# Kernel optimization log

Measured on AMD Instinct MI355X. Metric: run time of the kernel, lower is better.

## Reference

```python
import jax, jax.numpy as jnp
import numpy as np
from jax import lax

B = 8
N = 460800          # anchors per image
PRE = 2000          # pre_nms_top_n
POST = 1000         # post_nms_top_n
NMS_T = 0.7
MIN_SIZE = 1e-3
IMG_H = 1024.0
IMG_W = 1024.0
BBOX_XFORM_CLIP = float(np.log(1000.0 / 16.0))


def setup_inputs() -> dict:
    key = jax.random.key(0)
    k1, k2, k3, k4 = jax.random.split(key, 4)
    # plausible anchors: centers in image, sizes 16..256
    ctr = jax.random.uniform(k1, (N, 2), minval=0.0, maxval=1024.0)
    wh = jax.random.uniform(k2, (N, 2), minval=16.0, maxval=256.0)
    anchors = jnp.concatenate([ctr - 0.5 * wh, ctr + 0.5 * wh], axis=-1)
    objectness = jax.random.normal(k3, (B, N), dtype=jnp.float32)
    bbox_deltas = jax.random.normal(k4, (B, N, 4), dtype=jnp.float32) * 0.1
    return {"anchors": anchors, "objectness": objectness, "bbox_deltas": bbox_deltas}


def _decode(deltas, anchors):
    # BoxCoder.decode with weights (1,1,1,1)
    w = anchors[..., 2] - anchors[..., 0]
    h = anchors[..., 3] - anchors[..., 1]
    cx = anchors[..., 0] + 0.5 * w
    cy = anchors[..., 1] + 0.5 * h
    dx, dy = deltas[..., 0], deltas[..., 1]
    dw = jnp.minimum(deltas[..., 2], BBOX_XFORM_CLIP)
    dh = jnp.minimum(deltas[..., 3], BBOX_XFORM_CLIP)
    pcx = dx * w + cx
    pcy = dy * h + cy
    pw = jnp.exp(dw) * w
    ph = jnp.exp(dh) * h
    return jnp.stack([pcx - 0.5 * pw, pcy - 0.5 * ph,
                      pcx + 0.5 * pw, pcy + 0.5 * ph], axis=-1)


def _nms_keep(boxes, valid):
    # boxes: [PRE,4] sorted by descending score; greedy NMS keep mask
    area = (boxes[:, 2] - boxes[:, 0]) * (boxes[:, 3] - boxes[:, 1])
    lt = jnp.maximum(boxes[:, None, :2], boxes[None, :, :2])
    rb = jnp.minimum(boxes[:, None, 2:], boxes[None, :, 2:])
    whi = jnp.clip(rb - lt, 0.0)
    inter = whi[..., 0] * whi[..., 1]          # [PRE,PRE]
    iou = inter / (area[:, None] + area[None, :] - inter)
    idx = jnp.arange(PRE)

    def body(i, keep):
        sup = keep[i] & (iou[i] > NMS_T) & (idx > i)
        return keep & ~sup

    return lax.fori_loop(0, PRE, body, valid)


def _per_image(proposals, scores):
    # top pre_nms_top_n by raw objectness (returned sorted descending)
    top_scores, idx = lax.top_k(scores, PRE)
    b = proposals[idx]                          # [PRE,4]
    # clip to image
    x1 = jnp.clip(b[:, 0], 0.0, IMG_W)
    y1 = jnp.clip(b[:, 1], 0.0, IMG_H)
    x2 = jnp.clip(b[:, 2], 0.0, IMG_W)
    y2 = jnp.clip(b[:, 3], 0.0, IMG_H)
    b = jnp.stack([x1, y1, x2, y2], axis=-1)
    # remove small boxes (mask instead of drop, jit-friendly)
    small = (x2 - x1 < MIN_SIZE) | (y2 - y1 < MIN_SIZE)
    keep = _nms_keep(b, ~small)
    s = jnp.where(keep, top_scores, -jnp.inf)
    _, fidx = lax.top_k(s, POST)
    return b[fidx]                              # [POST,4]


def reference(anchors, objectness, bbox_deltas):
    proposals = _decode(bbox_deltas, anchors[None])   # [B,N,4]
    boxes = jax.vmap(_per_image)(proposals, objectness)  # [B,POST,4]
    return boxes
```

## Files before the change

kernel.cpp:

```cpp
#include <hip/hip_runtime.h>
#include <stdint.h>

#define B 8
#define N 460800
#define NV4 115200
#define PRE 2000
#define POST 1000
#define CAP 4096
#define NBIN 4096
#define RANKP 2048
#define NWORD 32
#define NMS_T 0.7f
#define XCLIP 4.135166556742356

#define SCAN_BLOCKS 45
#define SCAN_ITER 10
#define SCAN_STRIDE (SCAN_BLOCKS * 256)

typedef unsigned long long u64;

__device__ __forceinline__ uint32_t fkey(float f) {
    uint32_t u = __float_as_uint(f);
    return (u & 0x80000000u) ? ~u : (u | 0x80000000u);
}

__device__ __forceinline__ u64 readlane_u64(u64 v, int lane) {
    uint32_t lo = __builtin_amdgcn_readlane((uint32_t)v, lane);
    uint32_t hi = __builtin_amdgcn_readlane((uint32_t)(v >> 32), lane);
    return ((u64)hi << 32) | lo;
}

#define ZBYTES 131328
__global__ __launch_bounds__(256) void k_zero(uint4* __restrict__ p) {
    int i = blockIdx.x * 256 + threadIdx.x;
    if (i < ZBYTES / 16) p[i] = make_uint4(0u, 0u, 0u, 0u);
}

__global__ __launch_bounds__(256) void k_hist(const float4* __restrict__ obj4,
                                              uint32_t* __restrict__ hist) {
    __shared__ uint32_t lh[2][NBIN];
    int b = blockIdx.y;
    for (int i = threadIdx.x; i < NBIN; i += 256) { lh[0][i] = 0; lh[1][i] = 0; }
    __syncthreads();
    const float4* s = obj4 + (size_t)b * NV4;
    int t0 = blockIdx.x * 256 + threadIdx.x;
    uint32_t* h = lh[threadIdx.x & 1];
    float4 v[SCAN_ITER];
#pragma unroll
    for (int k = 0; k < SCAN_ITER; ++k) v[k] = s[t0 + k * SCAN_STRIDE];
#pragma unroll
    for (int k = 0; k < SCAN_ITER; ++k) {
        atomicAdd(&h[fkey(v[k].x) >> 20], 1u);
        atomicAdd(&h[fkey(v[k].y) >> 20], 1u);
        atomicAdd(&h[fkey(v[k].z) >> 20], 1u);
        atomicAdd(&h[fkey(v[k].w) >> 20], 1u);
    }
    __syncthreads();
    uint32_t* gh = hist + (size_t)b * NBIN;
    for (int i = threadIdx.x; i < NBIN; i += 256) {
        uint32_t s2 = lh[0][i] + lh[1][i];
        if (s2) atomicAdd(&gh[i], s2);
    }
}

#define LBUF 2048
__global__ __launch_bounds__(256) void k_compact(const float4* __restrict__ obj4,
                                                 const uint32_t* __restrict__ hist,
                                                 uint32_t* __restrict__ cnt,
                                                 u64* __restrict__ cand) {
    __shared__ u64 buf[LBUF];
    __shared__ uint32_t lcnt, base, cutsh;
    int b = blockIdx.y;
    if (threadIdx.x == 0) lcnt = 0;
    if (threadIdx.x < 64) {
        int lane = threadIdx.x;
        const uint32_t* h = hist + (size_t)b * NBIN;
        uint32_t gs = 0;
        for (int t = 0; t < 64; ++t) gs += h[lane * 64 + t];
        uint32_t suf = gs;
        for (int d = 1; d < 64; d <<= 1) {
            uint32_t vv = __shfl_down(suf, d);
            if (lane + d < 64) suf += vv;
        }
        unsigned long long m = __ballot(suf >= PRE);
        int G = 63 - __clzll(m);
        uint32_t A = 0;
        if (G < 63) A = __shfl(suf, G + 1);
        uint32_t hv = h[G * 64 + lane];
        uint32_t suf2 = hv;
        for (int d = 1; d < 64; d <<= 1) {
            uint32_t vv = __shfl_down(suf2, d);
            if (lane + d < 64) suf2 += vv;
        }
        unsigned long long m2 = __ballot(A + suf2 >= PRE);
        int t2 = 63 - __clzll(m2);
        if (lane == 0) cutsh = (uint32_t)(G * 64 + t2);
    }
    __syncthreads();
    uint32_t cb = cutsh;
    const float4* s = obj4 + (size_t)b * NV4;
    int t0 = blockIdx.x * 256 + threadIdx.x;
    float4 v[SCAN_ITER];
#pragma unroll
    for (int k = 0; k < SCAN_ITER; ++k) v[k] = s[t0 + k * SCAN_STRIDE];
#pragma unroll
    for (int k = 0; k < SCAN_ITER; ++k) {
        int i4 = (t0 + k * SCAN_STRIDE) * 4;
        float fv[4] = {v[k].x, v[k].y, v[k].z, v[k].w};
#pragma unroll
        for (int c = 0; c < 4; ++c) {
            uint32_t key = fkey(fv[c]);
            if ((key >> 20) >= cb) {
                uint32_t p = atomicAdd(&lcnt, 1u);
                u64 e = ((u64)key << 32) | (uint32_t)(~(uint32_t)(i4 + c));
                if (p < LBUF) buf[p] = e;
                else {
                    uint32_t g = atomicAdd(&cnt[b], 1u);
                    if (g < CAP) cand[(size_t)b * CAP + g] = e;
                }
            }
        }
    }
    __syncthreads();
    uint32_t nb = lcnt < LBUF ? lcnt : LBUF;
    if (threadIdx.x == 0) base = atomicAdd(&cnt[b], nb);
    __syncthreads();
    uint32_t bs = base;
    for (uint32_t t = threadIdx.x; t < nb; t += 256) {
        uint32_t g = bs + t;
        if (g < CAP) cand[(size_t)b * CAP + g] = buf[t];
    }
}

__global__ __launch_bounds__(64) void k_rankdec(const uint32_t* __restrict__ cnt,
                                                const u64* __restrict__ cand,
                                                const float4* __restrict__ anchors,
                                                const float4* __restrict__ deltas,
                                                float4* __restrict__ boxes,
                                                uint32_t* __restrict__ occ) {
    int b = blockIdx.x;
    int lane = threadIdx.x;
    int slot = blockIdx.y * 64 + lane;
    uint32_t n = cnt[b]; if (n > CAP) n = CAP;
    const u64* C = cand + (size_t)b * CAP;
    u64 mykey = (slot < (int)n) ? C[slot] : 0ull;
    int ng = ((int)n + 63) >> 6;
    auto ld = [&](int g) -> u64 {
        int j = g * 64 + lane;
        int jc = j < (CAP - 1) ? j : (CAP - 1);
        u64 kv = C[jc];
        return (j < (int)n) ? kv : 0ull;
    };
    u64 kv0 = ld(0), kv1 = ld(1), kv2 = ld(2);
    int r0 = 0, r1 = 0;
    for (int g = 0; g < ng; ++g) {
        u64 kvn = ld(g + 3);
#pragma unroll
        for (int t = 0; t < 64; t += 2) {
            u64 ka = readlane_u64(kv0, t);
            u64 kb = readlane_u64(kv0, t + 1);
            r0 += (ka > mykey) ? 1 : 0;
            r1 += (kb > mykey) ? 1 : 0;
        }
        kv0 = kv1; kv1 = kv2; kv2 = kvn;
    }
    int r = r0 + r1;
    int rank = (slot < (int)n) ? r : slot;
    if (rank < RANKP) {
        float4 outb = make_float4(0.f, 0.f, 0.f, 0.f);
        if (slot < (int)n && rank < PRE) {
            uint32_t idx = ~(uint32_t)mykey;
            if (idx < N) {
                float4 a = anchors[idx];
                float4 d = deltas[(size_t)b * N + idx];
                float w = a.z - a.x, h = a.w - a.y;
                float cx = a.x + 0.5f * w, cy = a.y + 0.5f * h;
                float dw = fminf(d.z, (float)XCLIP);
                float dh = fminf(d.w, (float)XCLIP);
                float pcx = d.x * w + cx, pcy = d.y * h + cy;
                float pw = expf(dw) * w, ph = expf(dh) * h;
                float x1 = pcx - 0.5f * pw, y1 = pcy - 0.5f * ph;
                float x2 = pcx + 0.5f * pw, y2 = pcy + 0.5f * ph;
                x1 = fminf(fmaxf(x1, 0.f), 1024.f);
                y1 = fminf(fmaxf(y1, 0.f), 1024.f);
                x2 = fminf(fmaxf(x2, 0.f), 1024.f);
                y2 = fminf(fmaxf(y2, 0.f), 1024.f);
                outb = make_float4(x1, y1, x2, y2);
            }
        }
        boxes[(size_t)b * RANKP + rank] = outb;
        occ[(size_t)b * RANKP + rank] = 0u;
    }
}

#define NTRI (NWORD * (NWORD + 1) / 2)
__global__ void k_mask(const float4* __restrict__ boxes, u64* __restrict__ adj,
                       uint32_t* __restrict__ occ, u64* __restrict__ valid) {
    int b = blockIdx.x;
    int L = blockIdx.y;
    int tw = 0, rem = L;
    while (rem >= NWORD - tw) { rem -= NWORD - tw; ++tw; }
    int tr = tw + rem;
    __shared__ float4 jb[64];
    __shared__ float ja[64];
    int t = threadIdx.x;
    const float4* bx = boxes + (size_t)b * RANKP;
    float4 v = bx[tw * 64 + t];
    jb[t] = v;
    ja[t] = (v.z - v.x) * (v.w - v.y);
    int i = tr * 64 + t;
    float4 bi = bx[i];
    float ai = (bi.z - bi.x) * (bi.w - bi.y);
    __syncthreads();
    u64 word = 0;
    for (int kk = 0; kk < 64; ++kk) {
        int j = tw * 64 + kk;
        float4 bj = jb[kk];
        float xx1 = fmaxf(bi.x, bj.x), yy1 = fmaxf(bi.y, bj.y);
        float xx2 = fminf(bi.z, bj.z), yy2 = fminf(bi.w, bj.w);
        float iw = fmaxf(xx2 - xx1, 0.f), ih = fmaxf(yy2 - yy1, 0.f);
        float inter = iw * ih;
        float iou = inter / (ai + ja[kk] - inter);
        if (j < i && iou > NMS_T) word |= 1ull << kk;
    }
    __builtin_nontemporal_store(word, &adj[((size_t)b * RANKP + i) * NWORD + tw]);
    if (word) atomicOr(&occ[(size_t)b * RANKP + i], 1u << tw);
    if (tw == tr) {
        bool ok = !((bi.z - bi.x < 1e-3f) || (bi.w - bi.y < 1e-3f));
        u64 bal = __ballot(ok);
        if (t == 0) valid[(size_t)b * NWORD + tr] = bal;
    }
}

__global__ __launch_bounds__(64, 1) void k_nms(const u64* __restrict__ valid,
                                               const u64* __restrict__ adj,
                                               const uint32_t* __restrict__ occ,
                                               const float4* __restrict__ boxes,
                                               float4* __restrict__ out) {
    int b = blockIdx.x;
    int lane = threadIdx.x;
    const u64* AdjG = adj + (size_t)b * RANKP * NWORD;
    const uint32_t* OccG = occ + (size_t)b * RANKP;
    uint32_t o[NWORD];
#pragma unroll
    for (int g = 0; g < NWORD; ++g) o[g] = OccG[g * 64 + lane];
    u64 vw = (lane < 32) ? valid[(size_t)b * NWORD + lane] : 0ull;
    u64 t1[NWORD];
#pragma unroll
    for (int g = 0; g < NWORD; ++g) {
        uint32_t m = o[g];
        int w1 = m ? (int)__builtin_ctz(m) : 0;
        t1[g] = AdjG[(size_t)(g * 64 + lane) * NWORD + w1];
    }
    u64 kw = vw;
    int kcnt = 0;
    bool done = false;
#pragma unroll
    for (int c = 0; c < NWORD; ++c) {
        if (!done) {
            u64 om = __ballot(o[c] != 0);
            u64 vmask = readlane_u64(vw, c);
            u64 kc;
            if (om == 0ull) {
                kc = vmask;
            } else {
                kc = vmask & ~om;
                u64 mm = om;
                while (mm) {
                    int i = (int)__builtin_ctzll(mm); mm &= mm - 1;
                    uint32_t occv = __builtin_amdgcn_readlane(o[c], i);
                    bool suppressed = false;
                    uint32_t m2 = occv;
                    int w = (int)__builtin_ctz(m2); m2 &= m2 - 1;
                    u64 arow = readlane_u64(t1[c], i);
                    u64 ks = (w == c) ? kc : readlane_u64(kw, w);
                    if (arow & ks) suppressed = true;
                    while (m2 && !suppressed) {
                        w = (int)__builtin_ctz(m2); m2 &= m2 - 1;
                        u64 a2 = AdjG[(size_t)(c * 64 + i) * NWORD + w];
                        ks = (w == c) ? kc : readlane_u64(kw, w);
                        if (a2 & ks) suppressed = true;
                    }
                    if (((vmask >> i) & 1ull) && !suppressed) kc |= 1ull << i;
                }
            }
            if (lane == c) kw = kc;
            kcnt += (int)__popcll(kc);
            if (kcnt >= POST) done = true;
        }
    }
    int tot = 0;
    for (int ww = 0; ww < NWORD; ++ww)
        tot += (int)__popcll(readlane_u64(kw, ww));
    u64 below = (1ull << lane) - 1ull;
    int kcum = 0, ucum = 0;
    for (int ww = 0; ww < NWORD; ++ww) {
        u64 kv = readlane_u64(kw, ww);
        int pc = (int)__popcll(kv);
        bool kp = (kv >> lane) & 1ull;
        int pos;
        if (kp) pos = kcum + (int)__popcll(kv & below);
        else    pos = tot + ucum + (int)__popcll((~kv) & below);
        if (pos < POST) out[(size_t)b * POST + pos] = boxes[(size_t)b * RANKP + ww * 64 + lane];
        kcum += pc;
        ucum += 64 - pc;
    }
}

extern "C" void kernel_launch(void* const* d_in, const int* in_sizes, int n_in,
                              void* d_out, int out_size, void* d_ws, size_t ws_size,
                              hipStream_t stream) {
    const float* anchors = (const float*)d_in[0];
    const float* obj     = (const float*)d_in[1];
    const float* deltas  = (const float*)d_in[2];
    char* ws = (char*)d_ws;

    uint32_t* hist   = (uint32_t*)(ws + 0);
    uint32_t* cnt    = (uint32_t*)(ws + 131072);
    uint32_t* occ    = (uint32_t*)(ws + 131328);
    u64*      cand   = (u64*)(ws + 196864);
    float4*   boxes  = (float4*)(ws + 459008);
    u64*      valid  = (u64*)(ws + 983296);
    u64*      adj    = (u64*)(ws + 985344);

    k_zero<<<(ZBYTES / 16 + 255) / 256, 256, 0, stream>>>((uint4*)ws);

    dim3 gscan(SCAN_BLOCKS, B);
    k_hist<<<gscan, 256, 0, stream>>>((const float4*)obj, hist);
    k_compact<<<gscan, 256, 0, stream>>>((const float4*)obj, hist, cnt, cand);
    dim3 grank(B, CAP / 64);
    k_rankdec<<<grank, 64, 0, stream>>>(cnt, cand, (const float4*)anchors,
                                        (const float4*)deltas, boxes, occ);
    dim3 gmask(B, NTRI);
    k_mask<<<gmask, 64, 0, stream>>>(boxes, adj, occ, valid);
    k_nms<<<B, 64, 0, stream>>>(valid, adj, occ, boxes, (float4*)d_out);
}
```

Measured before the change: 89.94 us.

## Fuse mask and NMS kernels via last-block counter; split rank scan across two waves

The IoU mask kernel and the greedy NMS kernel are merged. Each mask block increments a per-image done counter, and the last block to finish runs the NMS for that image, which removes one kernel launch and its drain gap. The rank kernel now uses two waves per block that each count half the candidate groups and combine their partial ranks through shared memory, and blocks made entirely of padding skip the scan. Adjacency stores become ordinary stores so the fused NMS reads them from cache, at the cost of thread fences and a serial tail that now runs inside one block of the mask grid.

```diff
diff --git a/kernel.cpp b/kernel.cpp
--- a/kernel.cpp
+++ b/kernel.cpp
@@ -16,6 +16,7 @@
 #define SCAN_BLOCKS 45
 #define SCAN_ITER 10
 #define SCAN_STRIDE (SCAN_BLOCKS * 256)
+#define NTRI (NWORD * (NWORD + 1) / 2)
 
 typedef unsigned long long u64;
 
@@ -30,7 +31,7 @@
     return ((u64)hi << 32) | lo;
 }
 
-#define ZBYTES 131328
+#define ZBYTES 131360
 __global__ __launch_bounds__(256) void k_zero(uint4* __restrict__ p) {
     int i = blockIdx.x * 256 + threadIdx.x;
     if (i < ZBYTES / 16) p[i] = make_uint4(0u, 0u, 0u, 0u);
@@ -132,70 +133,86 @@
     }
 }
 
-__global__ __launch_bounds__(64) void k_rankdec(const uint32_t* __restrict__ cnt,
-                                                const u64* __restrict__ cand,
-                                                const float4* __restrict__ anchors,
-                                                const float4* __restrict__ deltas,
-                                                float4* __restrict__ boxes,
-                                                uint32_t* __restrict__ occ) {
+__global__ __launch_bounds__(128) void k_rankdec(const uint32_t* __restrict__ cnt,
+                                                 const u64* __restrict__ cand,
+                                                 const float4* __restrict__ anchors,
+                                                 const float4* __restrict__ deltas,
+                                                 float4* __restrict__ boxes,
+                                                 uint32_t* __restrict__ occ) {
+    __shared__ uint32_t rpart[64];
     int b = blockIdx.x;
-    int lane = threadIdx.x;
+    int tid = threadIdx.x;
+    int wid = tid >> 6, lane = tid & 63;
     int slot = blockIdx.y * 64 + lane;
     uint32_t n = cnt[b]; if (n > CAP) n = CAP;
     const u64* C = cand + (size_t)b * CAP;
     u64 mykey = (slot < (int)n) ? C[slot] : 0ull;
-    int ng = ((int)n + 63) >> 6;
-    auto ld = [&](int g) -> u64 {
-        int j = g * 64 + lane;
-        int jc = j < (CAP - 1) ? j : (CAP - 1);
-        u64 kv = C[jc];
-        return (j < (int)n) ? kv : 0ull;
-    };
-    u64 kv0 = ld(0), kv1 = ld(1), kv2 = ld(2);
-    int r0 = 0, r1 = 0;
-    for (int g = 0; g < ng; ++g) {
-        u64 kvn = ld(g + 3);
-#pragma unroll
-        for (int t = 0; t < 64; t += 2) {
-            u64 ka = readlane_u64(kv0, t);
-            u64 kb = readlane_u64(kv0, t + 1);
-            r0 += (ka > mykey) ? 1 : 0;
-            r1 += (kb > mykey) ? 1 : 0;
-        }
-        kv0 = kv1; kv1 = kv2; kv2 = kvn;
-    }
-    int r = r0 + r1;
-    int rank = (slot < (int)n) ? r : slot;
-    if (rank < RANKP) {
-        float4 outb = make_float4(0.f, 0.f, 0.f, 0.f);
-        if (slot < (int)n && rank < PRE) {
-            uint32_t idx = ~(uint32_t)mykey;
-            if (idx < N) {
-                float4 a = anchors[idx];
-                float4 d = deltas[(size_t)b * N + idx];
-                float w = a.z - a.x, h = a.w - a.y;
-                float cx = a.x + 0.5f * w, cy = a.y + 0.5f * h;
-                float dw = fminf(d.z, (float)XCLIP);
-                float dh = fminf(d.w, (float)XCLIP);
-                float pcx = d.x * w + cx, pcy = d.y * h + cy;
-                float pw = expf(dw) * w, ph = expf(dh) * h;
-                float x1 = pcx - 0.5f * pw, y1 = pcy - 0.5f * ph;
-                float x2 = pcx + 0.5f * pw, y2 = pcy + 0.5f * ph;
-                x1 = fminf(fmaxf(x1, 0.f), 1024.f);
-                y1 = fminf(fmaxf(y1, 0.f), 1024.f);
-                x2 = fminf(fmaxf(x2, 0.f), 1024.f);
-                y2 = fminf(fmaxf(y2, 0.f), 1024.f);
-                outb = make_float4(x1, y1, x2, y2);
+    int r = 0;
+    bool allpad = (blockIdx.y * 64 >= (int)n);
+    if (!allpad) {
+        int ng = ((int)n + 63) >> 6;
+        int g0 = wid ? (ng >> 1) : 0;
+        int g1 = wid ? ng : (ng >> 1);
+        auto ld = [&](int g) -> u64 {
+            int j = g * 64 + lane;
+            int jc = j < (CAP - 1) ? j : (CAP - 1);
+            u64 kv = C[jc];
+            return (j < (int)n) ? kv : 0ull;
+        };
+        u64 kv0 = ld(g0), kv1 = ld(g0 + 1), kv2 = ld(g0 + 2);
+        int r0 = 0, r1 = 0;
+        for (int g = g0; g < g1; ++g) {
+            u64 kvn = ld(g + 3);
+#pragma unroll
+            for (int t = 0; t < 64; t += 2) {
+                u64 ka = readlane_u64(kv0, t);
+                u64 kb = readlane_u64(kv0, t + 1);
+                r0 += (ka > mykey) ? 1 : 0;
+                r1 += (kb > mykey) ? 1 : 0;
             }
-        }
-        boxes[(size_t)b * RANKP + rank] = outb;
-        occ[(size_t)b * RANKP + rank] = 0u;
-    }
-}
-
-#define NTRI (NWORD * (NWORD + 1) / 2)
-__global__ void k_mask(const float4* __restrict__ boxes, u64* __restrict__ adj,
-                       uint32_t* __restrict__ occ, u64* __restrict__ valid) {
+            kv0 = kv1; kv1 = kv2; kv2 = kvn;
+        }
+        r = r0 + r1;
+    }
+    if (wid == 1) rpart[lane] = (uint32_t)r;
+    __syncthreads();
+    if (wid == 0) {
+        r += (int)rpart[lane];
+        int rank = (slot < (int)n) ? r : slot;
+        if (rank < RANKP) {
+            float4 outb = make_float4(0.f, 0.f, 0.f, 0.f);
+            if (slot < (int)n && rank < PRE) {
+                uint32_t idx = ~(uint32_t)mykey;
+                if (idx < N) {
+                    float4 a = anchors[idx];
+                    float4 d = deltas[(size_t)b * N + idx];
+                    float w = a.z - a.x, h = a.w - a.y;
+                    float cx = a.x + 0.5f * w, cy = a.y + 0.5f * h;
+                    float dw = fminf(d.z, (float)XCLIP);
+                    float dh = fminf(d.w, (float)XCLIP);
+                    float pcx = d.x * w + cx, pcy = d.y * h + cy;
+                    float pw = expf(dw) * w, ph = expf(dh) * h;
+                    float x1 = pcx - 0.5f * pw, y1 = pcy - 0.5f * ph;
+                    float x2 = pcx + 0.5f * pw, y2 = pcy + 0.5f * ph;
+                    x1 = fminf(fmaxf(x1, 0.f), 1024.f);
+                    y1 = fminf(fmaxf(y1, 0.f), 1024.f);
+                    x2 = fminf(fmaxf(x2, 0.f), 1024.f);
+                    y2 = fminf(fmaxf(y2, 0.f), 1024.f);
+                    outb = make_float4(x1, y1, x2, y2);
+                }
+            }
+            boxes[(size_t)b * RANKP + rank] = outb;
+            occ[(size_t)b * RANKP + rank] = 0u;
+        }
+    }
+}
+
+__global__ __launch_bounds__(64) void k_masknms(const float4* __restrict__ boxes,
+                                                u64* __restrict__ adj,
+                                                uint32_t* __restrict__ occ,
+                                                u64* __restrict__ valid,
+                                                uint32_t* __restrict__ done,
+                                                float4* __restrict__ out) {
     int b = blockIdx.x;
     int L = blockIdx.y;
     int tw = 0, rem = L;
@@ -203,12 +220,13 @@
     int tr = tw + rem;
     __shared__ float4 jb[64];
     __shared__ float ja[64];
-    int t = threadIdx.x;
+    __shared__ uint32_t oldv;
+    int lane = threadIdx.x;
     const float4* bx = boxes + (size_t)b * RANKP;
-    float4 v = bx[tw * 64 + t];
-    jb[t] = v;
-    ja[t] = (v.z - v.x) * (v.w - v.y);
-    int i = tr * 64 + t;
+    float4 v = bx[tw * 64 + lane];
+    jb[lane] = v;
+    ja[lane] = (v.z - v.x) * (v.w - v.y);
+    int i = tr * 64 + lane;
     float4 bi = bx[i];
     float ai = (bi.z - bi.x) * (bi.w - bi.y);
     __syncthreads();
@@ -223,22 +241,18 @@
         float iou = inter / (ai + ja[kk] - inter);
         if (j < i && iou > NMS_T) word |= 1ull << kk;
     }
-    __builtin_nontemporal_store(word, &adj[((size_t)b * RANKP + i) * NWORD + tw]);
+    adj[((size_t)b * RANKP + i) * NWORD + tw] = word;
     if (word) atomicOr(&occ[(size_t)b * RANKP + i], 1u << tw);
     if (tw == tr) {
         bool ok = !((bi.z - bi.x < 1e-3f) || (bi.w - bi.y < 1e-3f));
         u64 bal = __ballot(ok);
-        if (t == 0) valid[(size_t)b * NWORD + tr] = bal;
-    }
-}
-
-__global__ __launch_bounds__(64, 1) void k_nms(const u64* __restrict__ valid,
-                                               const u64* __restrict__ adj,
-                                               const uint32_t* __restrict__ occ,
-                                               const float4* __restrict__ boxes,
-                                               float4* __restrict__ out) {
-    int b = blockIdx.x;
-    int lane = threadIdx.x;
+        if (lane == 0) valid[(size_t)b * NWORD + tr] = bal;
+    }
+    __threadfence();
+    if (lane == 0) oldv = atomicAdd(&done[b], 1u);
+    __syncthreads();
+    if (oldv != NTRI - 1) return;
+    __threadfence();
     const u64* AdjG = adj + (size_t)b * RANKP * NWORD;
     const uint32_t* OccG = occ + (size_t)b * RANKP;
     uint32_t o[NWORD];
@@ -254,10 +268,10 @@
     }
     u64 kw = vw;
     int kcnt = 0;
-    bool done = false;
+    bool fin = false;
 #pragma unroll
     for (int c = 0; c < NWORD; ++c) {
-        if (!done) {
+        if (!fin) {
             u64 om = __ballot(o[c] != 0);
             u64 vmask = readlane_u64(vw, c);
             u64 kc;
@@ -267,26 +281,26 @@
                 kc = vmask & ~om;
                 u64 mm = om;
                 while (mm) {
-                    int i = (int)__builtin_ctzll(mm); mm &= mm - 1;
-                    uint32_t occv = __builtin_amdgcn_readlane(o[c], i);
+                    int ii = (int)__builtin_ctzll(mm); mm &= mm - 1;
+                    uint32_t occv = __builtin_amdgcn_readlane(o[c], ii);
                     bool suppressed = false;
                     uint32_t m2 = occv;
                     int w = (int)__builtin_ctz(m2); m2 &= m2 - 1;
-                    u64 arow = readlane_u64(t1[c], i);
+                    u64 arow = readlane_u64(t1[c], ii);
                     u64 ks = (w == c) ? kc : readlane_u64(kw, w);
                     if (arow & ks) suppressed = true;
                     while (m2 && !suppressed) {
                         w = (int)__builtin_ctz(m2); m2 &= m2 - 1;
-                        u64 a2 = AdjG[(size_t)(c * 64 + i) * NWORD + w];
+                        u64 a2 = AdjG[(size_t)(c * 64 + ii) * NWORD + w];
                         ks = (w == c) ? kc : readlane_u64(kw, w);
                         if (a2 & ks) suppressed = true;
                     }
-                    if (((vmask >> i) & 1ull) && !suppressed) kc |= 1ull << i;
+                    if (((vmask >> ii) & 1ull) && !suppressed) kc |= 1ull << ii;
                 }
             }
             if (lane == c) kw = kc;
             kcnt += (int)__popcll(kc);
-            if (kcnt >= POST) done = true;
+            if (kcnt >= POST) fin = true;
         }
     }
     int tot = 0;
@@ -317,11 +331,12 @@
 
     uint32_t* hist   = (uint32_t*)(ws + 0);
     uint32_t* cnt    = (uint32_t*)(ws + 131072);
-    uint32_t* occ    = (uint32_t*)(ws + 131328);
-    u64*      cand   = (u64*)(ws + 196864);
-    float4*   boxes  = (float4*)(ws + 459008);
-    u64*      valid  = (u64*)(ws + 983296);
-    u64*      adj    = (u64*)(ws + 985344);
+    uint32_t* done   = (uint32_t*)(ws + 131328);
+    uint32_t* occ    = (uint32_t*)(ws + 131584);
+    u64*      cand   = (u64*)(ws + 197120);
+    float4*   boxes  = (float4*)(ws + 459264);
+    u64*      valid  = (u64*)(ws + 983552);
+    u64*      adj    = (u64*)(ws + 985600);
 
     k_zero<<<(ZBYTES / 16 + 255) / 256, 256, 0, stream>>>((uint4*)ws);
 
@@ -329,9 +344,8 @@
     k_hist<<<gscan, 256, 0, stream>>>((const float4*)obj, hist);
     k_compact<<<gscan, 256, 0, stream>>>((const float4*)obj, hist, cnt, cand);
     dim3 grank(B, CAP / 64);
-    k_rankdec<<<grank, 64, 0, stream>>>(cnt, cand, (const float4*)anchors,
-                                        (const float4*)deltas, boxes, occ);
+    k_rankdec<<<grank, 128, 0, stream>>>(cnt, cand, (const float4*)anchors,
+                                         (const float4*)deltas, boxes, occ);
     dim3 gmask(B, NTRI);
-    k_mask<<<gmask, 64, 0, stream>>>(boxes, adj, occ, valid);
-    k_nms<<<B, 64, 0, stream>>>(valid, adj, occ, boxes, (float4*)d_out);
-}
+    k_masknms<<<gmask, 64, 0, stream>>>(boxes, adj, occ, valid, done, (float4*)d_out);
+}
```

Measured after the change: 198.3 us. 2.21x slower.
